# Optimization experiments

Hardware: AMD Instinct MI355X
Metric: run time of the kernel (lower is better)

## Reference

```python
import jax, jax.numpy as jnp
import numpy as np

B, S, H = 4, 4096, 1024
NUM_LEVELS, DECAY = 3, 0.8
D0, D1 = 512, 204  # int(1024*0.5), int(512*0.5*0.8)


def _xavier(key, shape):
    fan_in, fan_out = shape
    return jax.random.normal(key, shape, dtype=jnp.float32) * np.sqrt(2.0 / (fan_in + fan_out))


def setup_inputs() -> dict:
    key = jax.random.key(0)
    ks = jax.random.split(key, 8)
    return {
        "keys": jax.random.normal(ks[0], (B, S, H), dtype=jnp.float32),
        "values": jax.random.normal(ks[1], (B, S, H), dtype=jnp.float32),
        "importance": jax.random.uniform(ks[2], (B, S), dtype=jnp.float32),
        # encoder layers (stored as [in, out]; torch Linear applies x @ W.T + b)
        "We0": _xavier(ks[3], (H, D0)), "be0": jnp.zeros((D0,), jnp.float32),
        "We1": _xavier(ks[4], (D0, D1)), "be1": jnp.zeros((D1,), jnp.float32),
        # decoder layers
        "Wd0": _xavier(ks[5], (D0, H)), "bd0": jnp.zeros((H,), jnp.float32),
        "Wd1": _xavier(ks[6], (D1, D0)), "bd1": jnp.zeros((D0,), jnp.float32),
    }


def _level_sizes(n):
    sizes, remaining = [], n
    for i in range(NUM_LEVELS):
        if i == NUM_LEVELS - 1:
            sizes.append(remaining)
        else:
            sz = int(remaining * (1 - DECAY) * DECAY ** i)
            sizes.append(sz)
            remaining -= sz
    return sizes


def reference(keys, values, importance, We0, be0, We1, be1, Wd0, bd0, Wd1, bd1):
    n = B * S
    fk = keys.reshape(n, H)
    fv = values.reshape(n, H)
    sorted_idx = jnp.argsort(-importance.reshape(-1))  # descending importance
    sizes = _level_sizes(n)

    def chain(x, level):
        # encode 0..level-1 with ReLU, then decode level-1..0 with ReLU
        if level >= 1:
            x = jax.nn.relu(x @ We0 + be0)
        if level >= 2:
            x = jax.nn.relu(x @ We1 + be1)
            x = jax.nn.relu(x @ Wd1 + bd1)
        if level >= 1:
            x = jax.nn.relu(x @ Wd0 + bd0)
        return x

    ck = jnp.zeros_like(fk)
    cv = jnp.zeros_like(fv)
    start = 0
    for level, size in enumerate(sizes):
        if size <= 0:
            continue
        idx = jax.lax.dynamic_slice(sorted_idx, (start,), (size,))
        ck = ck.at[idx].set(chain(fk[idx], level))
        cv = cv.at[idx].set(chain(fv[idx], level))
        start += size
    return ck.reshape(B, S, H), cv.reshape(B, S, H)
```

## Files before the change

### kernel.cpp

```cpp
#include <hip/hip_runtime.h>

typedef __attribute__((ext_vector_type(8))) short short8;
typedef __attribute__((ext_vector_type(4))) float f32x4;

#define N_TOK   16384
#define HDIM    1024
#define OUT_OFF 16777216
#define M1ROWS  26216
#define M2ROWS  22022
#define L2ROW0  4194

__device__ __forceinline__ unsigned short f2bf(float f) {
  unsigned int u = __float_as_uint(f);
  u += 0x7FFFu + ((u >> 16) & 1u);
  return (unsigned short)(u >> 16);
}

__device__ __forceinline__ void rowmap(int r, int& is_v, int& rank) {
  if (r < 2097)       { is_v = 0; rank = 3276 + r; }
  else if (r < 4194)  { is_v = 1; rank = 1179 + r; }
  else if (r < 15205) { is_v = 0; rank = 1179 + r; }
  else                { is_v = 1; rank = r - 9832; }
}

__global__ __launch_bounds__(256) void rank_count(const float* __restrict__ imp,
                                                  int* __restrict__ counts) {
  __shared__ float sj[2048];
  const int i = blockIdx.x * 256 + threadIdx.x;
  const int jbase = blockIdx.y * 2048;
  const float vi = imp[i];
  for (int s = threadIdx.x; s < 2048; s += 256) sj[s] = imp[jbase + s];
  __syncthreads();
  int cnt = 0;
  #pragma unroll 8
  for (int s = 0; s < 2048; ++s) {
    float vj = sj[s];
    bool gt = vj > vi;
    bool eq = (vj == vi) && ((jbase + s) < i);
    cnt += (gt || eq) ? 1 : 0;
  }
  atomicAdd(&counts[i], cnt);
}

__global__ __launch_bounds__(256) void scatter_order(const int* __restrict__ counts,
                                                     int* __restrict__ order) {
  int i = blockIdx.x * 256 + threadIdx.x;
  order[counts[i]] = i;
}

__global__ __launch_bounds__(256) void wconv(unsigned short* __restrict__ dst,
                                             const float* __restrict__ src,
                                             int Nd, int Kd, int Nsrc, int Ksrc) {
  int idx = blockIdx.x * 256 + threadIdx.x;
  if (idx >= Nd * Kd) return;
  int n = idx / Kd, k = idx % Kd;
  float v = (n < Nsrc && k < Ksrc) ? src[k * Nsrc + n] : 0.f;
  dst[idx] = f2bf(v);
}

__global__ __launch_bounds__(256) void gather_rows(unsigned short* __restrict__ X,
                                                   const float* __restrict__ keys,
                                                   const float* __restrict__ values,
                                                   const int* __restrict__ order) {
  int r = blockIdx.x;
  int is_v, rank; rowmap(r, is_v, rank);
  int token = order[rank];
  const float* src = (is_v ? values : keys) + (size_t)token * HDIM;
  int c = threadIdx.x * 4;
  float4 f = *reinterpret_cast<const float4*>(src + c);
  ushort4 h;
  h.x = f2bf(f.x); h.y = f2bf(f.y); h.z = f2bf(f.z); h.w = f2bf(f.w);
  *reinterpret_cast<ushort4*>(X + (size_t)r * HDIM + c) = h;
}

__global__ __launch_bounds__(256) void copy_level0(float* __restrict__ out,
                                                   const float* __restrict__ keys,
                                                   const float* __restrict__ values,
                                                   const int* __restrict__ order) {
  int b = blockIdx.x;
  int is_v = b & 1, rank = b >> 1;
  int token = order[rank];
  const float* src = (is_v ? values : keys) + (size_t)token * HDIM;
  float* dst = out + (is_v ? OUT_OFF : 0) + (size_t)token * HDIM;
  int c = threadIdx.x * 4;
  *reinterpret_cast<float4*>(dst + c) = *reinterpret_cast<const float4*>(src + c);
}

#define GLDS16(g, l) __builtin_amdgcn_global_load_lds( \
    (const __attribute__((address_space(1))) void*)(g), \
    (__attribute__((address_space(3))) void*)(l), 16, 0, 0)

template<int MODE>
__global__ __launch_bounds__(256) void gemm_bias_relu(
    const unsigned short* __restrict__ A, int M, int K,
    const unsigned short* __restrict__ Bt, int N,
    const float* __restrict__ bias, int Nbias,
    unsigned short* __restrict__ Cbf, int ldc,
    float* __restrict__ outf, const int* __restrict__ order) {
  __shared__ __align__(16) unsigned short As[2][128 * 32];
  __shared__ __align__(16) unsigned short Bs[2][128 * 32];
  const int tid = threadIdx.x;
  const int wave = tid >> 6, lane = tid & 63;
  const int row0 = blockIdx.x * 128, col0 = blockIdx.y * 128;
  const int lrow = lane >> 2;
  const int lk = (((lane & 3) ^ ((lane >> 3) & 3)) << 3);
  const int wr = (wave >> 1) * 64, wc = (wave & 1) * 64;

  const int s0 = wave * 2, s1 = wave * 2 + 1;
  int ar0 = row0 + s0 * 16 + lrow; if (ar0 >= M) ar0 = 0;
  int ar1 = row0 + s1 * 16 + lrow; if (ar1 >= M) ar1 = 0;
  int br0 = col0 + s0 * 16 + lrow; if (br0 >= N) br0 = 0;
  int br1 = col0 + s1 * 16 + lrow; if (br1 >= N) br1 = 0;
  const unsigned short* ap0 = A + (size_t)ar0 * K + lk;
  const unsigned short* ap1 = A + (size_t)ar1 * K + lk;
  const unsigned short* bp0 = Bt + (size_t)br0 * K + lk;
  const unsigned short* bp1 = Bt + (size_t)br1 * K + lk;

  f32x4 acc[4][4] = {};
  const int fr = lane & 15;
  const int qoff = (((lane >> 4) ^ ((fr >> 1) & 3)) << 3);

  const int nt = K >> 5;
  GLDS16(ap0, As[0] + s0 * 512);
  GLDS16(ap1, As[0] + s1 * 512);
  GLDS16(bp0, Bs[0] + s0 * 512);
  GLDS16(bp1, Bs[0] + s1 * 512);
  __syncthreads();

  int cur = 0;
  for (int t = 0; t < nt; ++t) {
    if (t + 1 < nt) {
      const int k1 = (t + 1) << 5;
      GLDS16(ap0 + k1, As[cur ^ 1] + s0 * 512);
      GLDS16(ap1 + k1, As[cur ^ 1] + s1 * 512);
      GLDS16(bp0 + k1, Bs[cur ^ 1] + s0 * 512);
      GLDS16(bp1 + k1, Bs[cur ^ 1] + s1 * 512);
    }
    const unsigned short* as = As[cur];
    const unsigned short* bs = Bs[cur];
    short8 af[4], bfv[4];
    #pragma unroll
    for (int m = 0; m < 4; ++m)
      af[m] = *reinterpret_cast<const short8*>(as + (wr + m * 16 + fr) * 32 + qoff);
    #pragma unroll
    for (int n = 0; n < 4; ++n)
      bfv[n] = *reinterpret_cast<const short8*>(bs + (wc + n * 16 + fr) * 32 + qoff);
    #pragma unroll
    for (int m = 0; m < 4; ++m)
      #pragma unroll
      for (int n = 0; n < 4; ++n)
        acc[m][n] = __builtin_amdgcn_mfma_f32_16x16x32_bf16(af[m], bfv[n], acc[m][n], 0, 0, 0);
    __syncthreads();
    cur ^= 1;
  }

  const int orow = (lane >> 4) * 4;
  const int ocol = lane & 15;
  #pragma unroll
  for (int m = 0; m < 4; ++m) {
    #pragma unroll
    for (int n = 0; n < 4; ++n) {
      #pragma unroll
      for (int j = 0; j < 4; ++j) {
        int r = row0 + wr + m * 16 + orow + j;
        int c = col0 + wc + n * 16 + ocol;
        if (r < M && c < N) {
          float v = acc[m][n][j] + (c < Nbias ? bias[c] : 0.f);
          v = fmaxf(v, 0.f);
          if (MODE == 0) {
            Cbf[(size_t)r * ldc + c] = f2bf(v);
          } else {
            int iv, rk; rowmap(r, iv, rk);
            int token = order[rk];
            outf[(size_t)(iv ? OUT_OFF : 0) + (size_t)token * HDIM + c] = v;
          }
        }
      }
    }
  }
}

extern "C" void kernel_launch(void* const* d_in, const int* in_sizes, int n_in,
                              void* d_out, int out_size, void* d_ws, size_t ws_size,
                              hipStream_t stream) {
  const float* keys   = (const float*)d_in[0];
  const float* values = (const float*)d_in[1];
  const float* imp    = (const float*)d_in[2];
  const float* We0    = (const float*)d_in[3];
  const float* be0    = (const float*)d_in[4];
  const float* We1    = (const float*)d_in[5];
  const float* be1    = (const float*)d_in[6];
  const float* Wd0    = (const float*)d_in[7];
  const float* bd0    = (const float*)d_in[8];
  const float* Wd1    = (const float*)d_in[9];
  const float* bd1    = (const float*)d_in[10];

  char* ws = (char*)d_ws;
  int* counts           = (int*)(ws);
  int* order            = (int*)(ws + 65536);
  unsigned short* We0T  = (unsigned short*)(ws + 131072);
  unsigned short* We1T  = (unsigned short*)(ws + 1179648);
  unsigned short* Wd1T  = (unsigned short*)(ws + 1409024);
  unsigned short* Wd0T  = (unsigned short*)(ws + 1638400);
  unsigned short* Y     = (unsigned short*)(ws + 2686976);
  unsigned short* Z     = (unsigned short*)(ws + 29532160);
  unsigned short* X = (unsigned short*)d_out;
  float* outf = (float*)d_out;

  hipMemsetAsync(counts, 0, 65536, stream);
  rank_count<<<dim3(64, 8), 256, 0, stream>>>(imp, counts);
  scatter_order<<<64, 256, 0, stream>>>(counts, order);

  wconv<<<2048, 256, 0, stream>>>(We0T, We0, 512, 1024, 512, 1024);
  wconv<<<448,  256, 0, stream>>>(We1T, We1, 224, 512, 204, 512);
  wconv<<<448,  256, 0, stream>>>(Wd1T, Wd1, 512, 224, 512, 204);
  wconv<<<2048, 256, 0, stream>>>(Wd0T, Wd0, 1024, 512, 1024, 512);

  gather_rows<<<M1ROWS, 256, 0, stream>>>(X, keys, values, order);

  gemm_bias_relu<0><<<dim3(205, 4), 256, 0, stream>>>(
      X, M1ROWS, 1024, We0T, 512, be0, 512, Y, 512, nullptr, nullptr);

  copy_level0<<<6552, 256, 0, stream>>>(outf, keys, values, order);

  gemm_bias_relu<0><<<dim3(173, 2), 256, 0, stream>>>(
      Y + (size_t)L2ROW0 * 512, M2ROWS, 512, We1T, 224, be1, 204, Z, 224, nullptr, nullptr);

  gemm_bias_relu<0><<<dim3(173, 4), 256, 0, stream>>>(
      Z, M2ROWS, 224, Wd1T, 512, bd1, 512, Y + (size_t)L2ROW0 * 512, 512, nullptr, nullptr);

  gemm_bias_relu<1><<<dim3(205, 8), 256, 0, stream>>>(
      Y, M1ROWS, 512, Wd0T, 1024, bd0, 1024, nullptr, 0, outf, order);
}
```

Baseline: 330.9 us.

## Triple-buffer GEMM LDS pipeline and swizzle block order for cache reuse

The GEMM kernel moves from double to triple-buffered LDS tiles. Loads run two k-steps ahead, and explicit vmcnt waits plus one barrier per iteration replace the two __syncthreads calls. Launches become a 1D grid remapped so groups of 8 row-tiles share column tiles, which should improve L2 reuse of A and B tiles. The cost is more LDS per block, which may lower occupancy, and the hand-written waitcnt logic depends on the compiler keeping the expected load counts.

```diff
diff --git a/kernel.cpp b/kernel.cpp
--- a/kernel.cpp
+++ b/kernel.cpp
@@ -96,12 +96,21 @@
     const unsigned short* __restrict__ Bt, int N,
     const float* __restrict__ bias, int Nbias,
     unsigned short* __restrict__ Cbf, int ldc,
-    float* __restrict__ outf, const int* __restrict__ order) {
-  __shared__ __align__(16) unsigned short As[2][128 * 32];
-  __shared__ __align__(16) unsigned short Bs[2][128 * 32];
+    float* __restrict__ outf, const int* __restrict__ order,
+    int NP, int NC) {
+  __shared__ __align__(16) unsigned short As[3][128 * 32];
+  __shared__ __align__(16) unsigned short Bs[3][128 * 32];
+  const int bid = blockIdx.x;
+  const int r8 = bid & 7;
+  const int rest = bid >> 3;
+  const int c8 = rest % NC;
+  const int q8 = rest / NC;
+  const int p8 = q8 * 8 + r8;
+  if (p8 >= NP) return;
+  const int row0 = p8 * 128, col0 = c8 * 128;
+
   const int tid = threadIdx.x;
   const int wave = tid >> 6, lane = tid & 63;
-  const int row0 = blockIdx.x * 128, col0 = blockIdx.y * 128;
   const int lrow = lane >> 2;
   const int lk = (((lane & 3) ^ ((lane >> 3) & 3)) << 3);
   const int wr = (wave >> 1) * 64, wc = (wave & 1) * 64;
@@ -125,17 +134,17 @@
   GLDS16(ap1, As[0] + s1 * 512);
   GLDS16(bp0, Bs[0] + s0 * 512);
   GLDS16(bp1, Bs[0] + s1 * 512);
-  __syncthreads();
+  GLDS16(ap0 + 32, As[1] + s0 * 512);
+  GLDS16(ap1 + 32, As[1] + s1 * 512);
+  GLDS16(bp0 + 32, Bs[1] + s0 * 512);
+  GLDS16(bp1 + 32, Bs[1] + s1 * 512);
 
   int cur = 0;
   for (int t = 0; t < nt; ++t) {
-    if (t + 1 < nt) {
-      const int k1 = (t + 1) << 5;
-      GLDS16(ap0 + k1, As[cur ^ 1] + s0 * 512);
-      GLDS16(ap1 + k1, As[cur ^ 1] + s1 * 512);
-      GLDS16(bp0 + k1, Bs[cur ^ 1] + s0 * 512);
-      GLDS16(bp1 + k1, Bs[cur ^ 1] + s1 * 512);
-    }
+    if (t + 1 < nt) asm volatile("s_waitcnt vmcnt(4)" ::: "memory");
+    else            asm volatile("s_waitcnt vmcnt(0)" ::: "memory");
+    __builtin_amdgcn_s_barrier();
+    __builtin_amdgcn_sched_barrier(0);
     const unsigned short* as = As[cur];
     const unsigned short* bs = Bs[cur];
     short8 af[4], bfv[4];
@@ -145,13 +154,20 @@
     #pragma unroll
     for (int n = 0; n < 4; ++n)
       bfv[n] = *reinterpret_cast<const short8*>(bs + (wc + n * 16 + fr) * 32 + qoff);
+    if (t + 2 < nt) {
+      const int k2 = (t + 2) << 5;
+      int nb = cur + 2; if (nb >= 3) nb -= 3;
+      GLDS16(ap0 + k2, As[nb] + s0 * 512);
+      GLDS16(ap1 + k2, As[nb] + s1 * 512);
+      GLDS16(bp0 + k2, Bs[nb] + s0 * 512);
+      GLDS16(bp1 + k2, Bs[nb] + s1 * 512);
+    }
     #pragma unroll
     for (int m = 0; m < 4; ++m)
       #pragma unroll
       for (int n = 0; n < 4; ++n)
         acc[m][n] = __builtin_amdgcn_mfma_f32_16x16x32_bf16(af[m], bfv[n], acc[m][n], 0, 0, 0);
-    __syncthreads();
-    cur ^= 1;
+    cur = (cur == 2) ? 0 : cur + 1;
   }
 
   const int orow = (lane >> 4) * 4;
@@ -180,6 +196,8 @@
   }
 }
 
+static inline int swz_grid(int NP, int NC) { return 8 * NC * ((NP + 7) / 8); }
+
 extern "C" void kernel_launch(void* const* d_in, const int* in_sizes, int n_in,
                               void* d_out, int out_size, void* d_ws, size_t ws_size,
                               hipStream_t stream) {
@@ -218,17 +236,19 @@
 
   gather_rows<<<M1ROWS, 256, 0, stream>>>(X, keys, values, order);
 
-  gemm_bias_relu<0><<<dim3(205, 4), 256, 0, stream>>>(
-      X, M1ROWS, 1024, We0T, 512, be0, 512, Y, 512, nullptr, nullptr);
+  gemm_bias_relu<0><<<swz_grid(205, 4), 256, 0, stream>>>(
+      X, M1ROWS, 1024, We0T, 512, be0, 512, Y, 512, nullptr, nullptr, 205, 4);
 
   copy_level0<<<6552, 256, 0, stream>>>(outf, keys, values, order);
 
-  gemm_bias_relu<0><<<dim3(173, 2), 256, 0, stream>>>(
-      Y + (size_t)L2ROW0 * 512, M2ROWS, 512, We1T, 224, be1, 204, Z, 224, nullptr, nullptr);
-
-  gemm_bias_relu<0><<<dim3(173, 4), 256, 0, stream>>>(
-      Z, M2ROWS, 224, Wd1T, 512, bd1, 512, Y + (size_t)L2ROW0 * 512, 512, nullptr, nullptr);
-
-  gemm_bias_relu<1><<<dim3(205, 8), 256, 0, stream>>>(
-      Y, M1ROWS, 512, Wd0T, 1024, bd0, 1024, nullptr, 0, outf, order);
-}
+  gemm_bias_relu<0><<<swz_grid(173, 2), 256, 0, stream>>>(
+      Y + (size_t)L2ROW0 * 512, M2ROWS, 512, We1T, 224, be1, 204, Z, 224,
+      nullptr, nullptr, 173, 2);
+
+  gemm_bias_relu<0><<<swz_grid(173, 4), 256, 0, stream>>>(
+      Z, M2ROWS, 224, Wd1T, 512, bd1, 512, Y + (size_t)L2ROW0 * 512, 512,
+      nullptr, nullptr, 173, 4);
+
+  gemm_bias_relu<1><<<swz_grid(205, 8), 256, 0, stream>>>(
+      Y, M1ROWS, 512, Wd0T, 1024, bd0, 1024, nullptr, 0, outf, order, 205, 8);
+}
```

Result: faster. 304.2 us (-8.1%).
